# Kernel optimization log

Measured on AMD Instinct MI355X. Metric: run time of the kernel, lower is better.

Reference implementation:

```python
import jax, jax.numpy as jnp
import numpy as np

H, M, K, V = 16, 1024, 64, 64
B, Q, T = 2, 2048, 2048


def masked_softmax(x, active, axis):
    # Matches jax.nn.softmax(x, axis=axis, where=active, initial=0.0):
    # max over active entries with an initial value of 0.0; inactive -> prob 0.
    m = jnp.max(jnp.where(active, x, -jnp.inf), axis=axis, keepdims=True)
    m = jnp.maximum(m, 0.0)  # initial=0.0
    e = jnp.where(active, jnp.exp(x - m), 0.0)
    return e / jnp.sum(e, axis=axis, keepdims=True)


def setup_inputs() -> dict:
    key = jax.random.key(0)
    k1, k2, k3, k4, k5, k6, k7 = jax.random.split(key, 7)
    mscale = 1.0 / np.sqrt(M)
    vscale = 1.0 / np.sqrt(V)
    return {
        "qinput": jax.random.normal(k1, (B, Q, M), jnp.float32),
        "kvinput": jax.random.normal(k2, (B, T, M), jnp.float32),
        "qtmask": jax.random.randint(k3, (B, Q, T), 0, 2, jnp.int32),
        "wq": jax.random.normal(k4, (H, M, K), jnp.float32) * mscale,
        "wk": jax.random.normal(k5, (H, M, K), jnp.float32) * mscale,
        "wv": jax.random.normal(k6, (H, M, V), jnp.float32) * mscale,
        "wo": jax.random.normal(k7, (H, V, M), jnp.float32) * vscale,
    }


def reference(qinput, kvinput, qtmask, wq, wk, wv, wo):
    kscale = 1.0 / np.sqrt(K)
    query = jnp.einsum('hmd,bqm->bhqd', wq, qinput)
    key_ = jnp.einsum('hmd,btm->bhtd', wk, kvinput)
    val = jnp.einsum('hmd,btm->bhtd', wv, kvinput)
    alogit = jnp.einsum('bhqd,bhtd->bhqt', query, key_)
    active = jnp.broadcast_to(jnp.logical_not(qtmask)[:, None, :, :], alogit.shape)
    att = masked_softmax(alogit * kscale, active, axis=3)  # bhqt
    pre = jnp.einsum('bhqt,bhtd->bhqd', att, val)
    out = jnp.einsum('hdm,bhqd->bqm', wo, pre)
    return (out, att)
```

## Files before the change

kernel.cpp:

```cpp
#include <hip/hip_runtime.h>

typedef _Float16 f16;
typedef __attribute__((ext_vector_type(2))) _Float16 f16x2;
typedef __attribute__((ext_vector_type(4))) _Float16 f16x4;
typedef __attribute__((ext_vector_type(8))) _Float16 f16x8;
typedef __attribute__((ext_vector_type(4))) float f32x4;

#define GLDS16(gp, lp)                                                        \
  __builtin_amdgcn_global_load_lds(                                           \
      (const __attribute__((address_space(1))) void*)(gp),                    \
      (__attribute__((address_space(3))) void*)(lp), 16, 0, 0)

__device__ __forceinline__ f32x4 mfma16(f16x8 a, f16x8 b, f32x4 c) {
  return __builtin_amdgcn_mfma_f32_16x16x32_f16(a, b, c, 0, 0, 0);
}

__global__ __launch_bounds__(256) void k_prep(
    const float* __restrict__ qin, const float* __restrict__ kvin,
    const int* __restrict__ qt, const float* __restrict__ wq,
    const float* __restrict__ wk, const float* __restrict__ wv,
    const float* __restrict__ wo, f16* __restrict__ Xq, f16* __restrict__ Xkv,
    unsigned* __restrict__ Mb, f16* __restrict__ WqT, f16* __restrict__ WkT,
    f16* __restrict__ WvT, f16* __restrict__ WoT) {
  __shared__ float tile[64][65];
  const int bx = blockIdx.x, tid = threadIdx.x;
  if (bx < 8192) {
    const float* s = bx < 4096 ? qin : kvin;
    f16* d = bx < 4096 ? Xq : Xkv;
    int i = ((bx & 4095) * 256 + tid) * 4;
    float4 v = *(const float4*)(s + i);
    f16x4 h;
    h[0] = (f16)v.x; h[1] = (f16)v.y; h[2] = (f16)v.z; h[3] = (f16)v.w;
    *(f16x4*)(d + i) = h;
    return;
  }
  if (bx < 9216) {
    int w = (bx - 8192) * 256 + tid;
    const int* p = qt + (long)w * 32;
    unsigned m = 0;
#pragma unroll
    for (int j4 = 0; j4 < 8; ++j4) {
      int4 v = *(const int4*)(p + j4 * 4);
      m |= (v.x == 0 ? 1u : 0u) << (j4 * 4 + 0);
      m |= (v.y == 0 ? 1u : 0u) << (j4 * 4 + 1);
      m |= (v.z == 0 ? 1u : 0u) << (j4 * 4 + 2);
      m |= (v.w == 0 ? 1u : 0u) << (j4 * 4 + 3);
    }
    Mb[w] = m;
    return;
  }
  int sgt = bx - 9216, which = sgt >> 8, t = sgt & 255;
  const float* src;
  f16* dst;
  int sldr, r0, c0;
  const int dldr = 1024;
  if (which == 0) {
    src = wq + (long)(t >> 4) * 65536; dst = WqT + (long)(t >> 4) * 65536;
    sldr = 64; r0 = (t & 15) * 64; c0 = 0;
  } else if (which == 1) {
    src = wk + (long)(t >> 4) * 65536; dst = WkT + (long)(t >> 4) * 65536;
    sldr = 64; r0 = (t & 15) * 64; c0 = 0;
  } else if (which == 2) {
    src = wv + (long)(t >> 4) * 65536; dst = WvT + (long)(t >> 4) * 65536;
    sldr = 64; r0 = (t & 15) * 64; c0 = 0;
  } else {
    src = wo; dst = WoT;
    sldr = 1024; r0 = (t >> 4) * 64; c0 = (t & 15) * 64;
  }
  int r = tid >> 2, cq = (tid & 3) * 16;
#pragma unroll
  for (int j = 0; j < 16; j += 4) {
    float4 v = *(const float4*)(src + (long)(r0 + r) * sldr + c0 + cq + j);
    tile[r][cq + j] = v.x; tile[r][cq + j + 1] = v.y;
    tile[r][cq + j + 2] = v.z; tile[r][cq + j + 3] = v.w;
  }
  __syncthreads();
  int c = tid >> 2, rq = (tid & 3) * 16;
  f16x8 h0, h1;
#pragma unroll
  for (int j = 0; j < 8; ++j) h0[j] = (f16)tile[rq + j][c];
#pragma unroll
  for (int j = 0; j < 8; ++j) h1[j] = (f16)tile[rq + 8 + j][c];
  f16* dp = dst + (long)(c0 + c) * dldr + r0 + rq;
  *(f16x8*)dp = h0;
  *(f16x8*)(dp + 8) = h1;
}

__device__ __forceinline__ void gemm_body(const f16* __restrict__ A,
                                          const f16* __restrict__ Bt,
                                          void* __restrict__ Cout, int Kd,
                                          int N, int bxx, int byy, int f32out,
                                          f16* Al, f16* Bl) {
  const int tid = threadIdx.x, l = tid & 63, w = tid >> 6;
  const int wm = w >> 1, wn = w & 1;
  const int m0 = byy * 128, n0 = bxx * 128;
  const int lr = l >> 2;
  const int lc = (l & 3) * 8;
  const int fr = l & 15;
  const int fk = (l >> 4) * 8;
  f32x4 acc[4][4] = {};
  for (int k0 = 0; k0 < Kd; k0 += 32) {
#pragma unroll
    for (int rd = 0; rd < 2; ++rd) {
      GLDS16(A + (long)(m0 + rd * 64 + w * 16 + lr) * Kd + k0 + lc,
             (char*)Al + rd * 4096 + w * 1024);
      GLDS16(Bt + (long)(n0 + rd * 64 + w * 16 + lr) * Kd + k0 + lc,
             (char*)Bl + rd * 4096 + w * 1024);
    }
    __syncthreads();
    f16x8 af[4], bf[4];
#pragma unroll
    for (int i = 0; i < 4; ++i) {
      af[i] = *(const f16x8*)(Al + (wm * 64 + i * 16 + fr) * 32 + fk);
      bf[i] = *(const f16x8*)(Bl + (wn * 64 + i * 16 + fr) * 32 + fk);
    }
#pragma unroll
    for (int i = 0; i < 4; ++i)
#pragma unroll
      for (int j = 0; j < 4; ++j)
        acc[i][j] = mfma16(af[i], bf[j], acc[i][j]);
    __syncthreads();
  }
  const int rb = (l >> 4) * 4;
#pragma unroll
  for (int i = 0; i < 4; ++i)
#pragma unroll
    for (int j = 0; j < 4; ++j) {
      int row = m0 + wm * 64 + i * 16 + rb;
      int col = n0 + wn * 64 + j * 16 + fr;
#pragma unroll
      for (int r = 0; r < 4; ++r) {
        if (f32out)
          ((float*)Cout)[(long)(row + r) * N + col] = acc[i][j][r];
        else
          ((f16*)Cout)[(long)(row + r) * N + col] = (f16)acc[i][j][r];
      }
    }
}

__global__ __launch_bounds__(256) void k_gemm_qkv(
    const f16* __restrict__ Xq, const f16* __restrict__ WqT,
    f16* __restrict__ Qm, const f16* __restrict__ Xkv,
    const f16* __restrict__ WkT, f16* __restrict__ KVm) {
  __shared__ __attribute__((aligned(16))) f16 Al[128 * 32];
  __shared__ __attribute__((aligned(16))) f16 Bl[128 * 32];
  if (blockIdx.x < 8)
    gemm_body(Xq, WqT, (void*)Qm, 1024, 1024, blockIdx.x, blockIdx.y, 0, Al,
              Bl);
  else
    gemm_body(Xkv, WkT, (void*)KVm, 1024, 2048, blockIdx.x - 8, blockIdx.y, 0,
              Al, Bl);
}

__global__ __launch_bounds__(256) void k_gemm_out(const f16* __restrict__ Pre,
                                                  const f16* __restrict__ WoT,
                                                  float* __restrict__ out) {
  __shared__ __attribute__((aligned(16))) f16 Al[128 * 32];
  __shared__ __attribute__((aligned(16))) f16 Bl[128 * 32];
  gemm_body(Pre, WoT, (void*)out, 1024, 1024, blockIdx.x, blockIdx.y, 1, Al,
            Bl);
}

__global__ __launch_bounds__(256) void k_vtr(const f16* __restrict__ KVm,
                                             f16* __restrict__ Vt) {
  const int z = blockIdx.z, b = z >> 4, cc = z & 15;
  const f16* src = KVm + (long)b * 4194304 + 1024 + cc * 64;
  f16* dst = Vt + (long)b * 2097152 + (long)cc * 131072;
  const int r0 = blockIdx.y * 64;
  __shared__ __attribute__((aligned(16))) f16 tile[64][80];
  const int t = threadIdx.x;
  int r = t >> 2, cq = (t & 3) * 16;
  *(f16x8*)&tile[r][cq] = *(const f16x8*)(src + (long)(r0 + r) * 2048 + cq);
  *(f16x8*)&tile[r][cq + 8] =
      *(const f16x8*)(src + (long)(r0 + r) * 2048 + cq + 8);
  __syncthreads();
  int c = t >> 2, rq = (t & 3) * 16;
  f16x8 h0, h1;
#pragma unroll
  for (int j = 0; j < 8; ++j) h0[j] = tile[rq + j][c];
#pragma unroll
  for (int j = 0; j < 8; ++j) h1[j] = tile[rq + 8 + j][c];
  f16* dp = dst + (long)c * 2048 + r0 + rq;
  *(f16x8*)dp = h0;
  *(f16x8*)(dp + 8) = h1;
}

__global__ __launch_bounds__(512, 4) void k_attn(
    const f16* __restrict__ Qm, const f16* __restrict__ Km,
    const f16* __restrict__ Vt, const unsigned* __restrict__ mb,
    float* __restrict__ att, f16* __restrict__ Pre, int ldk) {
  __shared__ unsigned mloc[32 * 68];
  __shared__ float wsum[8][16];
  __shared__ float rsum[32];
  __shared__ __attribute__((aligned(16))) f16 ebuf[8][16 * 136];
  const int qt = blockIdx.x, h = blockIdx.y, b = blockIdx.z;
  const int q0 = qt * 32;
  const int tid = threadIdx.x, l = tid & 63, w = tid >> 6;
  const int fr = l & 15, fg = l >> 4;
  const int qh = w & 1;
  const int ts = w >> 1;
  const int qrow = qh * 16 + fr;

  for (int i = tid; i < 2048; i += 512)
    mloc[(i >> 6) * 68 + (i & 63)] =
        mb[(long)(b * 2048 + q0 + (i >> 6)) * 64 + (i & 63)];

  const f16* qb = Qm + (long)(b * 2048 + q0 + qrow) * 1024 + h * 64 + fg * 8;
  f16x8 qf0 = *(const f16x8*)qb;
  f16x8 qf1 = *(const f16x8*)(qb + 32);
#pragma unroll
  for (int j = 0; j < 8; ++j) {
    qf0[j] *= (f16)0.18033688f;
    qf1[j] *= (f16)0.18033688f;
  }
  __syncthreads();

  const f16* kb = Km + (long)(b * 2048 + ts * 512 + fr) * ldk + h * 64 + fg * 8;
  f16x8 ka0[2], ka1[2];
#pragma unroll
  for (int p = 0; p < 2; ++p) {
    ka0[p] = *(const f16x8*)(kb + (long)p * 16 * ldk);
    ka1[p] = *(const f16x8*)(kb + (long)p * 16 * ldk + 32);
  }
  f16x4 s16[32];
  float sm[4] = {0.f, 0.f, 0.f, 0.f};
#pragma unroll
  for (int i = 0; i < 32; ++i) {
    f16x8 k0 = ka0[i & 1], k1 = ka1[i & 1];
    if (i < 30) {
      ka0[i & 1] = *(const f16x8*)(kb + (long)(i + 2) * 16 * ldk);
      ka1[i & 1] = *(const f16x8*)(kb + (long)(i + 2) * 16 * ldk + 32);
    }
    f32x4 s = {};
    s = mfma16(k0, qf0, s);
    s = mfma16(k1, qf1, s);
    unsigned bits =
        (mloc[qrow * 68 + ts * 16 + (i >> 1)] >> ((i & 1) * 16 + fg * 4)) &
        0xFu;
    f16x4 e4;
#pragma unroll
    for (int r = 0; r < 4; ++r) {
      float ev = ((bits >> r) & 1) ? __builtin_amdgcn_exp2f(s[r]) : 0.f;
      sm[r] += ev;
      e4[r] = (f16)ev;
    }
    s16[i] = e4;
  }
  float sa = (sm[0] + sm[1]) + (sm[2] + sm[3]);
  sa += __shfl_xor(sa, 16, 64);
  sa += __shfl_xor(sa, 32, 64);
  if (l < 16) wsum[w][fr] = sa;
  __syncthreads();
  float tot = (wsum[qh][fr] + wsum[qh + 2][fr]) +
              (wsum[qh + 4][fr] + wsum[qh + 6][fr]);
  float rinv = 1.f / tot;
  if (w < 2 && l < 16) rsum[qh * 16 + fr] = rinv;

  float* ao =
      att + (long)((b * 16 + h) * 2048 + q0 + qrow) * 2048 + ts * 512 + fg * 4;
#pragma unroll
  for (int i = 0; i < 32; ++i) {
    f16x4 e4 = s16[i];
    f32x4 o;
    o[0] = (float)e4[0] * rinv;
    o[1] = (float)e4[1] * rinv;
    o[2] = (float)e4[2] * rinv;
    o[3] = (float)e4[3] * rinv;
    __builtin_nontemporal_store(o, (f32x4*)(ao + i * 16));
  }

  f16* eb = ebuf[w];
  const f16* vb =
      Vt + ((long)((b * 16 + h) * 64 + fr)) * 2048 + ts * 512 + fg * 8;
  f32x4 pacc[4] = {};
#pragma unroll
  for (int c = 0; c < 4; ++c) {
#pragma unroll
    for (int i2 = 0; i2 < 8; ++i2)
      *(f16x4*)(eb + fr * 136 + i2 * 16 + fg * 4) = s16[c * 8 + i2];
#pragma unroll
    for (int kt = 0; kt < 4; ++kt) {
      f16x8 af = *(const f16x8*)(eb + fr * 136 + kt * 32 + fg * 8);
#pragma unroll
      for (int vt = 0; vt < 4; ++vt) {
        f16x8 bf =
            *(const f16x8*)(vb + (long)vt * 16 * 2048 + c * 128 + kt * 32);
        pacc[vt] = mfma16(af, bf, pacc[vt]);
      }
    }
  }

  float* pp = (float*)eb;
#pragma unroll
  for (int vt = 0; vt < 4; ++vt)
#pragma unroll
    for (int r = 0; r < 4; ++r)
      pp[(fg * 4 + r) * 64 + vt * 16 + fr] = pacc[vt][r];
  __syncthreads();
  {
    const int q = tid >> 4, v4 = (tid & 15) * 4;
    f32x4 p4 = {0.f, 0.f, 0.f, 0.f};
#pragma unroll
    for (int t4 = 0; t4 < 4; ++t4) {
      f32x4 u4 =
          *(const f32x4*)((const float*)ebuf[(q >> 4) + 2 * t4] +
                          (q & 15) * 64 + v4);
      p4 += u4;
    }
    float ri = rsum[q];
    f16x4 o;
    o[0] = (f16)(p4[0] * ri);
    o[1] = (f16)(p4[1] * ri);
    o[2] = (f16)(p4[2] * ri);
    o[3] = (f16)(p4[3] * ri);
    *(f16x4*)(Pre + (long)(b * 2048 + q0 + q) * 1024 + h * 64 + v4) = o;
  }
}

extern "C" void kernel_launch(void* const* d_in, const int* in_sizes, int n_in,
                              void* d_out, int out_size, void* d_ws,
                              size_t ws_size, hipStream_t stream) {
  const float* qinput = (const float*)d_in[0];
  const float* kvinput = (const float*)d_in[1];
  const int* qtmask = (const int*)d_in[2];
  const float* wq = (const float*)d_in[3];
  const float* wk = (const float*)d_in[4];
  const float* wv = (const float*)d_in[5];
  const float* wo = (const float*)d_in[6];
  float* out = (float*)d_out;
  float* att = out + (long)2 * 2048 * 1024;

  char* ws = (char*)d_ws;
  f16* Xq = (f16*)(ws);
  f16* Xkv = (f16*)(ws + 8388608);
  f16* WqT = (f16*)(ws + 16777216);
  f16* WkT = (f16*)(ws + 18874368);
  f16* WvT = (f16*)(ws + 20971520);
  f16* WoT = (f16*)(ws + 23068672);
  f16* Qm = (f16*)(ws + 25165824);
  f16* KVm = (f16*)(ws + 33554432);
  f16* Vt = (f16*)(ws + 50331648);
  f16* Pre = (f16*)(ws + 58720256);
  unsigned* Mb = (unsigned*)(ws + 67108864);

  k_prep<<<dim3(10240), dim3(256), 0, stream>>>(qinput, kvinput, qtmask, wq,
                                                wk, wv, wo, Xq, Xkv, Mb, WqT,
                                                WkT, WvT, WoT);
  k_gemm_qkv<<<dim3(24, 32), dim3(256), 0, stream>>>(Xq, WqT, Qm, Xkv, WkT,
                                                     KVm);
  k_vtr<<<dim3(1, 32, 32), dim3(256), 0, stream>>>(KVm, Vt);
  k_attn<<<dim3(64, 16, 2), dim3(512), 0, stream>>>(Qm, KVm, Vt, Mb, att, Pre,
                                                    2048);
  k_gemm_out<<<dim3(8, 32), dim3(256), 0, stream>>>(Pre, WoT, out);
}
```

Measured before the change: 429.8 us.

## Fuse V transpose into QKV GEMM epilogue and fold query scale into prep

```diff
diff --git a/kernel.cpp b/kernel.cpp
--- a/kernel.cpp
+++ b/kernel.cpp
@@ -1,7 +1,6 @@
 #include <hip/hip_runtime.h>
 
 typedef _Float16 f16;
-typedef __attribute__((ext_vector_type(2))) _Float16 f16x2;
 typedef __attribute__((ext_vector_type(4))) _Float16 f16x4;
 typedef __attribute__((ext_vector_type(8))) _Float16 f16x8;
 typedef __attribute__((ext_vector_type(4))) float f32x4;
@@ -27,10 +26,12 @@
   if (bx < 8192) {
     const float* s = bx < 4096 ? qin : kvin;
     f16* d = bx < 4096 ? Xq : Xkv;
+    const float sc = bx < 4096 ? 0.18033688f : 1.0f;
     int i = ((bx & 4095) * 256 + tid) * 4;
     float4 v = *(const float4*)(s + i);
     f16x4 h;
-    h[0] = (f16)v.x; h[1] = (f16)v.y; h[2] = (f16)v.z; h[3] = (f16)v.w;
+    h[0] = (f16)(v.x * sc); h[1] = (f16)(v.y * sc);
+    h[2] = (f16)(v.z * sc); h[3] = (f16)(v.w * sc);
     *(f16x4*)(d + i) = h;
     return;
   }
@@ -89,7 +90,7 @@
 __device__ __forceinline__ void gemm_body(const f16* __restrict__ A,
                                           const f16* __restrict__ Bt,
                                           void* __restrict__ Cout, int Kd,
-                                          int N, int bxx, int byy, int f32out,
+                                          int N, int bxx, int byy, int mode,
                                           f16* Al, f16* Bl) {
   const int tid = threadIdx.x, l = tid & 63, w = tid >> 6;
   const int wm = w >> 1, wn = w & 1;
@@ -128,12 +129,22 @@
     for (int j = 0; j < 4; ++j) {
       int row = m0 + wm * 64 + i * 16 + rb;
       int col = n0 + wn * 64 + j * 16 + fr;
-#pragma unroll
-      for (int r = 0; r < 4; ++r) {
-        if (f32out)
-          ((float*)Cout)[(long)(row + r) * N + col] = acc[i][j][r];
-        else
-          ((f16*)Cout)[(long)(row + r) * N + col] = (f16)acc[i][j][r];
+      if (mode == 2) {
+        int col2 = col - 1024;
+        long off = (long)(row >> 11) * 2097152 + (long)col2 * 2048 +
+                   (row & 2047);
+        f16x4 o;
+        o[0] = (f16)acc[i][j][0]; o[1] = (f16)acc[i][j][1];
+        o[2] = (f16)acc[i][j][2]; o[3] = (f16)acc[i][j][3];
+        *(f16x4*)((f16*)Cout + off) = o;
+      } else {
+#pragma unroll
+        for (int r = 0; r < 4; ++r) {
+          if (mode == 1)
+            ((float*)Cout)[(long)(row + r) * N + col] = acc[i][j][r];
+          else
+            ((f16*)Cout)[(long)(row + r) * N + col] = (f16)acc[i][j][r];
+        }
       }
     }
 }
@@ -141,15 +152,20 @@
 __global__ __launch_bounds__(256) void k_gemm_qkv(
     const f16* __restrict__ Xq, const f16* __restrict__ WqT,
     f16* __restrict__ Qm, const f16* __restrict__ Xkv,
-    const f16* __restrict__ WkT, f16* __restrict__ KVm) {
+    const f16* __restrict__ WkT, f16* __restrict__ KVm,
+    f16* __restrict__ Vt) {
   __shared__ __attribute__((aligned(16))) f16 Al[128 * 32];
   __shared__ __attribute__((aligned(16))) f16 Bl[128 * 32];
-  if (blockIdx.x < 8)
+  if (blockIdx.x < 8) {
     gemm_body(Xq, WqT, (void*)Qm, 1024, 1024, blockIdx.x, blockIdx.y, 0, Al,
               Bl);
-  else
-    gemm_body(Xkv, WkT, (void*)KVm, 1024, 2048, blockIdx.x - 8, blockIdx.y, 0,
-              Al, Bl);
+  } else {
+    int bxx = blockIdx.x - 8;
+    if (bxx < 8)
+      gemm_body(Xkv, WkT, (void*)KVm, 1024, 2048, bxx, blockIdx.y, 0, Al, Bl);
+    else
+      gemm_body(Xkv, WkT, (void*)Vt, 1024, 2048, bxx, blockIdx.y, 2, Al, Bl);
+  }
 }
 
 __global__ __launch_bounds__(256) void k_gemm_out(const f16* __restrict__ Pre,
@@ -161,31 +177,7 @@
             Bl);
 }
 
-__global__ __launch_bounds__(256) void k_vtr(const f16* __restrict__ KVm,
-                                             f16* __restrict__ Vt) {
-  const int z = blockIdx.z, b = z >> 4, cc = z & 15;
-  const f16* src = KVm + (long)b * 4194304 + 1024 + cc * 64;
-  f16* dst = Vt + (long)b * 2097152 + (long)cc * 131072;
-  const int r0 = blockIdx.y * 64;
-  __shared__ __attribute__((aligned(16))) f16 tile[64][80];
-  const int t = threadIdx.x;
-  int r = t >> 2, cq = (t & 3) * 16;
-  *(f16x8*)&tile[r][cq] = *(const f16x8*)(src + (long)(r0 + r) * 2048 + cq);
-  *(f16x8*)&tile[r][cq + 8] =
-      *(const f16x8*)(src + (long)(r0 + r) * 2048 + cq + 8);
-  __syncthreads();
-  int c = t >> 2, rq = (t & 3) * 16;
-  f16x8 h0, h1;
-#pragma unroll
-  for (int j = 0; j < 8; ++j) h0[j] = tile[rq + j][c];
-#pragma unroll
-  for (int j = 0; j < 8; ++j) h1[j] = tile[rq + 8 + j][c];
-  f16* dp = dst + (long)c * 2048 + r0 + rq;
-  *(f16x8*)dp = h0;
-  *(f16x8*)(dp + 8) = h1;
-}
-
-__global__ __launch_bounds__(512, 4) void k_attn(
+__global__ __launch_bounds__(512) void k_attn(
     const f16* __restrict__ Qm, const f16* __restrict__ Km,
     const f16* __restrict__ Vt, const unsigned* __restrict__ mb,
     float* __restrict__ att, f16* __restrict__ Pre, int ldk) {
@@ -208,11 +200,6 @@
   const f16* qb = Qm + (long)(b * 2048 + q0 + qrow) * 1024 + h * 64 + fg * 8;
   f16x8 qf0 = *(const f16x8*)qb;
   f16x8 qf1 = *(const f16x8*)(qb + 32);
-#pragma unroll
-  for (int j = 0; j < 8; ++j) {
-    qf0[j] *= (f16)0.18033688f;
-    qf1[j] *= (f16)0.18033688f;
-  }
   __syncthreads();
 
   const f16* kb = Km + (long)(b * 2048 + ts * 512 + fr) * ldk + h * 64 + fg * 8;
@@ -302,9 +289,8 @@
     f32x4 p4 = {0.f, 0.f, 0.f, 0.f};
 #pragma unroll
     for (int t4 = 0; t4 < 4; ++t4) {
-      f32x4 u4 =
-          *(const f32x4*)((const float*)ebuf[(q >> 4) + 2 * t4] +
-                          (q & 15) * 64 + v4);
+      f32x4 u4 = *(const f32x4*)((const float*)ebuf[(q >> 4) + 2 * t4] +
+                                 (q & 15) * 64 + v4);
       p4 += u4;
     }
     float ri = rsum[q];
@@ -347,8 +333,7 @@
                                                 wk, wv, wo, Xq, Xkv, Mb, WqT,
                                                 WkT, WvT, WoT);
   k_gemm_qkv<<<dim3(24, 32), dim3(256), 0, stream>>>(Xq, WqT, Qm, Xkv, WkT,
-                                                     KVm);
-  k_vtr<<<dim3(1, 32, 32), dim3(256), 0, stream>>>(KVm, Vt);
+                                                     KVm, Vt);
   k_attn<<<dim3(64, 16, 2), dim3(512), 0, stream>>>(Qm, KVm, Vt, Mb, att, Pre,
                                                     2048);
   k_gemm_out<<<dim3(8, 32), dim3(256), 0, stream>>>(Pre, WoT, out);
```

Result: faster. 376.4 us (-12.4%).
